# Performance work log

Hardware: AMD Instinct MI355X
Metric: run time of the kernel (lower is better)

## Reference

```python
import jax, jax.numpy as jnp
import numpy as np

D_MODEL = 1024
N_HEAD = 16
D_QKV = 64
B, L = 2, 2048
LN_EPS = 1e-5


def setup_inputs() -> dict:
    key = jax.random.key(0)
    ks = jax.random.split(key, 5)
    # xavier-normal-ish scale for [H, d_model, d_qkv] params
    std_in = (2.0 / (D_MODEL + D_QKV)) ** 0.5
    return {
        "x": jax.random.normal(ks[0], (B, L, D_MODEL), jnp.float32),
        "w_q": jax.random.normal(ks[1], (N_HEAD, D_MODEL, D_QKV), jnp.float32) * std_in,
        "w_k": jax.random.normal(ks[2], (N_HEAD, D_MODEL, D_QKV), jnp.float32) * std_in,
        "w_v": jax.random.normal(ks[3], (N_HEAD, D_MODEL, D_QKV), jnp.float32) * std_in,
        "w_o": jax.random.normal(ks[4], (N_HEAD, D_QKV, D_MODEL), jnp.float32) * std_in,
        "ln_gamma": jnp.ones((D_MODEL,), jnp.float32),
        "ln_beta": jnp.zeros((D_MODEL,), jnp.float32),
    }


def reference(x, w_q, w_k, w_v, w_o, ln_gamma, ln_beta):
    # q,k,v: [B, H, L, d_qkv]
    q = jnp.einsum('hmq,blm->bhlq', w_q, x)
    k = jnp.einsum('hmq,blm->bhlq', w_k, x)
    v = jnp.einsum('hmq,blm->bhlq', w_v, x)
    # scores: [B, H, L, L]
    s = jnp.einsum('bhiq,bhjq->bhij', q, k) / (D_QKV ** 0.5)
    s = jax.nn.softmax(s, axis=-1)
    # (dropout disabled: eval-mode reference)
    att = jnp.einsum('bhij,bhjq->bhiq', s, v)          # [B, H, L, d_qkv]
    out = jnp.einsum('bhlq,hqm->blm', att, w_o)        # [B, L, d_model]
    y = x + out                                        # residual
    mu = jnp.mean(y, axis=-1, keepdims=True)
    var = jnp.var(y, axis=-1, keepdims=True)
    return (y - mu) * jax.lax.rsqrt(var + LN_EPS) * ln_gamma + ln_beta
```

## Files before the change

### kernel.cpp

```cpp
#include <hip/hip_runtime.h>
#include <hip/hip_bf16.h>
#include <cstdint>

#define B_      2
#define L_      2048
#define DM_     1024
#define H_      16
#define DQ_     64
#define LN_EPS  1e-5f
#define QSCALE  0.1803368801111204f

typedef unsigned short u16;
typedef unsigned int   u32;
typedef __attribute__((ext_vector_type(8)))  short short8;
typedef __attribute__((ext_vector_type(4)))  unsigned short u16x4;
typedef __attribute__((ext_vector_type(4)))  unsigned int   u32x4;
typedef __attribute__((ext_vector_type(4)))  float f32x4;
typedef __attribute__((ext_vector_type(16))) float f32x16;

__device__ __forceinline__ u16 f2b(float f) {
  __hip_bfloat16 h = __float2bfloat16(f);
  return *reinterpret_cast<u16*>(&h);
}
__device__ __forceinline__ u32 pk2(float lo, float hi) {
  return (u32)f2b(lo) | ((u32)f2b(hi) << 16);
}

__device__ __forceinline__ void gl_lds16(const void* g, void* l) {
  auto gp = reinterpret_cast<const __attribute__((address_space(1))) unsigned int*>(
      reinterpret_cast<uintptr_t>(g));
  auto lp = reinterpret_cast<__attribute__((address_space(3))) unsigned int*>(
      reinterpret_cast<uintptr_t>(l));
  __builtin_amdgcn_global_load_lds(gp, lp, 16, 0, 0);
}

__device__ __forceinline__ short8 frag8(const u16* base, int row, int lchunk) {
  return *(const short8*)(base + row * 64 + ((lchunk ^ (row & 7)) << 3));
}

__global__ __launch_bounds__(256) void prep_all(
    const float* __restrict__ x, const float* __restrict__ wq,
    const float* __restrict__ wk, const float* __restrict__ wv,
    const float* __restrict__ wo, u16* __restrict__ xb,
    u16* __restrict__ wt, u16* __restrict__ wot) {
  __shared__ float Ls[64][65];
  const int t = threadIdx.x;
  const int bx = blockIdx.x;
  if (bx < 4096) {
    int i = bx * 256 + t;
    float4 v = ((const float4*)x)[i];
    u16x4 o = { f2b(v.x), f2b(v.y), f2b(v.z), f2b(v.w) };
    *(u16x4*)(xb + (size_t)i * 4) = o;
  } else if (bx < 4096 + 768) {
    int b2 = bx - 4096;
    int mt = b2 & 15, h = (b2 >> 4) & 15, wh = b2 >> 8;
    const float* in = ((wh == 0) ? wq : (wh == 1) ? wk : wv) + (size_t)h * DM_ * DQ_;
    #pragma unroll
    for (int i = 0; i < 16; ++i) {
      int idx = i * 256 + t, r = idx >> 6, c = idx & 63;
      Ls[r][c] = in[(size_t)(mt * 64 + r) * DQ_ + c];
    }
    __syncthreads();
    u16* outb = wt + (size_t)(wh * H_ + h) * DQ_ * DM_;
    #pragma unroll
    for (int i = 0; i < 16; ++i) {
      int idx = i * 256 + t, q = idx >> 6, mm = idx & 63;
      outb[(size_t)q * DM_ + mt * 64 + mm] = f2b(Ls[mm][q]);
    }
  } else {
    int b3 = bx - 4864;
    int mt = b3 & 15, kt = b3 >> 4;
    #pragma unroll
    for (int i = 0; i < 16; ++i) {
      int idx = i * 256 + t, r = idx >> 6, c = idx & 63;
      Ls[r][c] = wo[(size_t)(kt * 64 + r) * DM_ + mt * 64 + c];
    }
    __syncthreads();
    #pragma unroll
    for (int i = 0; i < 16; ++i) {
      int idx = i * 256 + t, mm = idx >> 6, kk = idx & 63;
      wot[(size_t)(mt * 64 + mm) * DM_ + kt * 64 + kk] = f2b(Ls[kk][mm]);
    }
  }
}

__global__ __launch_bounds__(256) void qkv_big(const u16* __restrict__ xb,
    const u16* __restrict__ wt, u16* __restrict__ Q, u16* __restrict__ K,
    u16* __restrict__ Vtg) {
  const int nt = blockIdx.x, mt = blockIdx.y;
  __shared__ __align__(16) u16 SH[128 * 136];
  u16* As_ = SH;
  u16* Bs_ = SH + 8192;
  const int t = threadIdx.x, w = t >> 6, lane = t & 63;
  const int lx = lane & 15, lq = lane >> 4;
  const int row0 = mt * 128, n0 = nt * 128;
  const int r8 = lane >> 3, lc = (lane & 7) ^ r8;
  const int wr = (w >> 1) * 64, wc = (w & 1) * 64;

  const u16* gA = xb + (size_t)(row0 + w * 32 + r8) * DM_ + lc * 8;
  const u16* gB = wt + (size_t)(n0  + w * 32 + r8) * DM_ + lc * 8;
  u16* lA = As_ + (w * 32) * 64;
  u16* lB = Bs_ + (w * 32) * 64;

  f32x4 z = {0.f, 0.f, 0.f, 0.f};
  f32x4 acc[4][4];
  #pragma unroll
  for (int mb = 0; mb < 4; ++mb)
    #pragma unroll
    for (int nb = 0; nb < 4; ++nb) acc[mb][nb] = z;

  for (int k0 = 0; k0 < DM_; k0 += 64) {
    #pragma unroll
    for (int i = 0; i < 4; ++i) {
      gl_lds16(gA + (size_t)i * 8 * DM_ + k0, lA + i * 8 * 64);
      gl_lds16(gB + (size_t)i * 8 * DM_ + k0, lB + i * 8 * 64);
    }
    __syncthreads();
    short8 af[4][2];
    #pragma unroll
    for (int mb = 0; mb < 4; ++mb)
      #pragma unroll
      for (int kh = 0; kh < 2; ++kh)
        af[mb][kh] = frag8(As_, wr + mb * 16 + lx, (kh << 2) | lq);
    #pragma unroll
    for (int nb = 0; nb < 4; ++nb) {
      short8 b0 = frag8(Bs_, wc + nb * 16 + lx, lq);
      short8 b1 = frag8(Bs_, wc + nb * 16 + lx, 4 | lq);
      #pragma unroll
      for (int mb = 0; mb < 4; ++mb) {
        acc[mb][nb] = __builtin_amdgcn_mfma_f32_16x16x32_bf16(af[mb][0], b0, acc[mb][nb], 0, 0, 0);
        acc[mb][nb] = __builtin_amdgcn_mfma_f32_16x16x32_bf16(af[mb][1], b1, acc[mb][nb], 0, 0, 0);
      }
    }
    __syncthreads();
  }

  const int wh = n0 >> 10;
  const float oscale = (wh == 0) ? QSCALE : 1.0f;
  const int bb = row0 >> 11, l0 = row0 & 2047;
  const int hd0 = n0 & 1023;
  u16* Ep = SH;

  if (wh != 2) {
    #pragma unroll
    for (int mb = 0; mb < 4; ++mb)
      #pragma unroll
      for (int nb = 0; nb < 4; ++nb)
        #pragma unroll
        for (int r = 0; r < 4; ++r) {
          int l = wr + mb * 16 + lq * 4 + r;
          Ep[l * 136 + wc + nb * 16 + lx] = f2b(acc[mb][nb][r] * oscale);
        }
    __syncthreads();
    u16* outp = (wh == 0) ? Q : K;
    #pragma unroll
    for (int hs = 0; hs < 2; ++hs) {
      const int hh = (hd0 >> 6) + hs;
      u16* gbase = outp + ((size_t)(bb * H_ + hh) * L_ + l0) * DQ_;
      #pragma unroll
      for (int it = 0; it < 4; ++it) {
        int u = it * 256 + t;
        int l = u >> 3, chunk = u & 7;
        *(uint4*)(gbase + u * 8) = *(const uint4*)&Ep[l * 136 + hs * 64 + chunk * 8];
      }
    }
  } else {
    #pragma unroll
    for (int mb = 0; mb < 4; ++mb)
      #pragma unroll
      for (int nb = 0; nb < 4; ++nb) {
        int l = wr + mb * 16 + lq * 4;
        int lp = (l & ~12) | ((l & 4) << 1) | ((l & 8) >> 1);
        uint2 pv = { pk2(acc[mb][nb][0], acc[mb][nb][1]),
                     pk2(acc[mb][nb][2], acc[mb][nb][3]) };
        *(uint2*)&Ep[(wc + nb * 16 + lx) * 136 + lp] = pv;
      }
    __syncthreads();
    #pragma unroll
    for (int it = 0; it < 8; ++it) {
      int v = it * 256 + t;
      int dloc = v >> 4, chunk = v & 15;
      int hh = (hd0 + dloc) >> 6, dd = (hd0 + dloc) & 63;
      u16* g = Vtg + ((size_t)(bb * H_ + hh) * DQ_ + dd) * L_ + l0 + chunk * 8;
      *(uint4*)g = *(const uint4*)&Ep[dloc * 136 + chunk * 8];
    }
  }
}

__global__ __launch_bounds__(512) void attn_mfma(const u16* __restrict__ Q,
    const u16* __restrict__ K, const u16* __restrict__ Vtg, u16* __restrict__ att) {
  const int ord = blockIdx.x;
  const int r_  = ord & 7, s_ = ord >> 3;
  const int qt  = s_ & 7, ghi = s_ >> 3;
  const int grp = r_ + 8 * ghi;
  const int h   = grp & 15, b = grp >> 4;
  __shared__ __align__(16) u16 Qs_[256 * 64];
  __shared__ __align__(16) u16 Ks_[2][64 * 64];
  __shared__ __align__(16) u16 Vt_[2][64 * 64];
  const int t = threadIdx.x, w = t >> 6, lane = t & 63;
  const int c = lane & 31, lsel = lane >> 5;
  const int r8 = lane >> 3, lc = (lane & 7) ^ r8;
  const size_t bh  = (size_t)(b * H_ + h) * L_ * DQ_;
  const size_t bhv = (size_t)(b * H_ + h) * DQ_ * L_;

  const u16* gQ = Q + bh + (size_t)(qt * 256 + w * 32 + r8) * DQ_ + lc * 8;
  #pragma unroll
  for (int i = 0; i < 4; ++i) gl_lds16(gQ + (size_t)i * 8 * DQ_, Qs_ + (w * 32 + i * 8) * 64);

  const u16* gK = K   + bh  + (size_t)(w * 8 + r8) * DQ_ + lc * 8;
  const u16* gV = Vtg + bhv + (size_t)(w * 8 + r8) * L_  + lc * 8;

  gl_lds16(gK, Ks_[0] + w * 8 * 64);
  gl_lds16(gV, Vt_[0] + w * 8 * 64);
  __syncthreads();
  short8 qb[4];
  #pragma unroll
  for (int km = 0; km < 4; ++km) qb[km] = frag8(Qs_, w * 32 + c, (km << 1) | lsel);

  f32x16 zz = {0.f,0.f,0.f,0.f,0.f,0.f,0.f,0.f,0.f,0.f,0.f,0.f,0.f,0.f,0.f,0.f};
  f32x16 oacc0 = zz, oacc1 = zz, lacc = zz;
  const short one_bf = (short)0x3F80;
  short8 ones = {one_bf, one_bf, one_bf, one_bf, one_bf, one_bf, one_bf, one_bf};

  for (int kt = 0; kt < L_ / 64; ++kt) {
    const int cur = kt & 1;
    __syncthreads();

    if (kt + 1 < L_ / 64) {
      const int nxt = 1 - cur;
      gl_lds16(gK + (size_t)(kt + 1) * 64 * DQ_, Ks_[nxt] + w * 8 * 64);
      gl_lds16(gV + (size_t)(kt + 1) * 64,       Vt_[nxt] + w * 8 * 64);
    }

    u32x4 paw[4];
    #pragma unroll
    for (int kb = 0; kb < 2; ++kb) {
      f32x16 s = zz;
      #pragma unroll
      for (int km = 0; km < 4; ++km) {
        short8 ka = frag8(Ks_[cur], kb * 32 + c, (km << 1) | lsel);
        s = __builtin_amdgcn_mfma_f32_32x32x16_bf16(ka, qb[km], s, 0, 0, 0);
      }
      #pragma unroll
      for (int F = 0; F < 2; ++F) {
        u32x4 pw;
        #pragma unroll
        for (int i = 0; i < 4; ++i) {
          float p0 = __builtin_amdgcn_exp2f(s[8 * F + 2 * i]);
          float p1 = __builtin_amdgcn_exp2f(s[8 * F + 2 * i + 1]);
          pw[i] = __builtin_amdgcn_perm(__float_as_uint(p1), __float_as_uint(p0), 0x07060302u);
        }
        paw[2 * kb + F] = pw;
      }
    }

    #pragma unroll
    for (int km = 0; km < 4; ++km) {
      short8 pa  = *reinterpret_cast<const short8*>(&paw[km]);
      short8 vb0 = frag8(Vt_[cur], c,      (km << 1) | lsel);
      short8 vb1 = frag8(Vt_[cur], 32 + c, (km << 1) | lsel);
      oacc0 = __builtin_amdgcn_mfma_f32_32x32x16_bf16(pa, vb0, oacc0, 0, 0, 0);
      oacc1 = __builtin_amdgcn_mfma_f32_32x32x16_bf16(pa, vb1, oacc1, 0, 0, 0);
      lacc  = __builtin_amdgcn_mfma_f32_32x32x16_bf16(pa, ones, lacc, 0, 0, 0);
    }
  }

  const int qrow_base = qt * 256 + w * 32;
  #pragma unroll
  for (int r = 0; r < 16; ++r) {
    int qr = (r & 3) + 8 * (r >> 2) + 4 * lsel;
    float inv = 1.0f / lacc[r];
    size_t base = (size_t)(b * L_ + qrow_base + qr) * DM_ + h * DQ_;
    att[base + c]      = f2b(oacc0[r] * inv);
    att[base + 32 + c] = f2b(oacc1[r] * inv);
  }
}

__global__ __launch_bounds__(256) void oproj_big(const u16* __restrict__ A,
    const u16* __restrict__ wot, float* __restrict__ out) {
  const int nt = blockIdx.x, mt = blockIdx.y;
  __shared__ __align__(16) u16 As_[128 * 64];
  __shared__ __align__(16) u16 Bs_[128 * 64];
  const int t = threadIdx.x, w = t >> 6, lane = t & 63;
  const int lx = lane & 15, lq = lane >> 4;
  const int row0 = mt * 128, n0 = nt * 128;
  const int r8 = lane >> 3, lc = (lane & 7) ^ r8;
  const int wr = (w >> 1) * 64, wc = (w & 1) * 64;

  const u16* gA = A   + (size_t)(row0 + w * 32 + r8) * DM_ + lc * 8;
  const u16* gB = wot + (size_t)(n0  + w * 32 + r8) * DM_ + lc * 8;
  u16* lA = As_ + (w * 32) * 64;
  u16* lB = Bs_ + (w * 32) * 64;

  f32x4 z = {0.f, 0.f, 0.f, 0.f};
  f32x4 acc[4][4];
  #pragma unroll
  for (int mb = 0; mb < 4; ++mb)
    #pragma unroll
    for (int nb = 0; nb < 4; ++nb) acc[mb][nb] = z;

  for (int k0 = 0; k0 < DM_; k0 += 64) {
    #pragma unroll
    for (int i = 0; i < 4; ++i) {
      gl_lds16(gA + (size_t)i * 8 * DM_ + k0, lA + i * 8 * 64);
      gl_lds16(gB + (size_t)i * 8 * DM_ + k0, lB + i * 8 * 64);
    }
    __syncthreads();
    short8 af[4][2];
    #pragma unroll
    for (int mb = 0; mb < 4; ++mb)
      #pragma unroll
      for (int kh = 0; kh < 2; ++kh)
        af[mb][kh] = frag8(As_, wr + mb * 16 + lx, (kh << 2) | lq);
    #pragma unroll
    for (int nb = 0; nb < 4; ++nb) {
      short8 b0 = frag8(Bs_, wc + nb * 16 + lx, lq);
      short8 b1 = frag8(Bs_, wc + nb * 16 + lx, 4 | lq);
      #pragma unroll
      for (int mb = 0; mb < 4; ++mb) {
        acc[mb][nb] = __builtin_amdgcn_mfma_f32_16x16x32_bf16(af[mb][0], b0, acc[mb][nb], 0, 0, 0);
        acc[mb][nb] = __builtin_amdgcn_mfma_f32_16x16x32_bf16(af[mb][1], b1, acc[mb][nb], 0, 0, 0);
      }
    }
    __syncthreads();
  }
  #pragma unroll
  for (int mb = 0; mb < 4; ++mb)
    #pragma unroll
    for (int nb = 0; nb < 4; ++nb)
      #pragma unroll
      for (int r = 0; r < 4; ++r) {
        int row = row0 + wr + mb * 16 + lq * 4 + r;
        out[(size_t)row * DM_ + n0 + wc + nb * 16 + lx] = acc[mb][nb][r];
      }
}

__global__ __launch_bounds__(256) void resid_ln(
    const float* __restrict__ x, const float* __restrict__ gamma,
    const float* __restrict__ beta, float* __restrict__ out) {
  const int row = blockIdx.x;
  const int t   = threadIdx.x;
  const float4* xp = (const float4*)(x   + (size_t)row * DM_);
  float4*       yp = (float4*)      (out + (size_t)row * DM_);

  float4 xv = xp[t];
  float4 av = yp[t];
  float y0 = xv.x + av.x, y1 = xv.y + av.y, y2 = xv.z + av.z, y3 = xv.w + av.w;

  float s  = y0 + y1 + y2 + y3;
  float s2 = y0 * y0 + y1 * y1 + y2 * y2 + y3 * y3;
  #pragma unroll
  for (int off = 32; off > 0; off >>= 1) {
    s  += __shfl_xor(s,  off, 64);
    s2 += __shfl_xor(s2, off, 64);
  }
  __shared__ float red[8];
  const int wave = t >> 6, lane = t & 63;
  if (lane == 0) { red[wave] = s; red[4 + wave] = s2; }
  __syncthreads();
  s  = red[0] + red[1] + red[2] + red[3];
  s2 = red[4] + red[5] + red[6] + red[7];

  const float mean = s * (1.f / DM_);
  const float var  = s2 * (1.f / DM_) - mean * mean;
  const float inv  = rsqrtf(var + LN_EPS);

  const float4 g  = ((const float4*)gamma)[t];
  const float4 bt = ((const float4*)beta)[t];
  float4 r;
  r.x = (y0 - mean) * inv * g.x + bt.x;
  r.y = (y1 - mean) * inv * g.y + bt.y;
  r.z = (y2 - mean) * inv * g.z + bt.z;
  r.w = (y3 - mean) * inv * g.w + bt.w;
  yp[t] = r;
}

extern "C" void kernel_launch(void* const* d_in, const int* in_sizes, int n_in,
                              void* d_out, int out_size, void* d_ws, size_t ws_size,
                              hipStream_t stream) {
  const float* x     = (const float*)d_in[0];
  const float* wq    = (const float*)d_in[1];
  const float* wk    = (const float*)d_in[2];
  const float* wv    = (const float*)d_in[3];
  const float* wo    = (const float*)d_in[4];
  const float* gamma = (const float*)d_in[5];
  const float* beta  = (const float*)d_in[6];
  float* out = (float*)d_out;

  char* ws = (char*)d_ws;
  u16* xb  = (u16*)ws;
  u16* Qb  = (u16*)(ws + ((size_t)8  << 20));
  u16* Kb  = (u16*)(ws + ((size_t)16 << 20));
  u16* Vtg = (u16*)(ws + ((size_t)24 << 20));
  u16* wt  = (u16*)(ws + ((size_t)32 << 20));
  u16* wot = (u16*)(ws + ((size_t)38 << 20));
  u16* att = (u16*)(ws + ((size_t)40 << 20));

  prep_all <<<5120, 256, 0, stream>>>(x, wq, wk, wv, wo, xb, wt, wot);
  qkv_big  <<<dim3(24, 32),    256, 0, stream>>>(xb, wt, Qb, Kb, Vtg);
  attn_mfma<<<256, 512, 0, stream>>>(Qb, Kb, Vtg, att);
  oproj_big<<<dim3(8, 32),     256, 0, stream>>>(att, wot, out);
  resid_ln <<<B_ * L_, 256, 0, stream>>>(x, gamma, beta, out);
}
```

Baseline: 186.3 us.

## Double-buffer QKV GEMM with 256x256 tiles, 512 threads and block swizzle

The QKV projection GEMM moves from 128x128 tiles with 256 threads and a single LDS buffer to 256x256 tiles with 512 threads and two LDS buffers. Global-to-LDS loads for the next K-step are issued during the MFMA work, synchronised with explicit vmcnt waits and raw s_barrier. A block-index swizzle is added for cache locality, and the epilogue is done in two halves to fit LDS. This aims to hide load latency and raise data reuse, at the cost of fewer blocks (192 on a 256-CU part), more registers per thread, and 128KB of LDS.

```diff
diff --git a/kernel.cpp b/kernel.cpp
--- a/kernel.cpp
+++ b/kernel.cpp
@@ -33,6 +33,8 @@
       reinterpret_cast<uintptr_t>(l));
   __builtin_amdgcn_global_load_lds(gp, lp, 16, 0, 0);
 }
+
+__device__ __forceinline__ void bar() { asm volatile("s_barrier" ::: "memory"); }
 
 __device__ __forceinline__ short8 frag8(const u16* base, int row, int lchunk) {
   return *(const short8*)(base + row * 64 + ((lchunk ^ (row & 7)) << 3));
@@ -84,105 +86,154 @@
   }
 }
 
-__global__ __launch_bounds__(256) void qkv_big(const u16* __restrict__ xb,
+__global__ __launch_bounds__(512) void qkv_big(const u16* __restrict__ xb,
     const u16* __restrict__ wt, u16* __restrict__ Q, u16* __restrict__ K,
     u16* __restrict__ Vtg) {
-  const int nt = blockIdx.x, mt = blockIdx.y;
-  __shared__ __align__(16) u16 SH[128 * 136];
-  u16* As_ = SH;
-  u16* Bs_ = SH + 8192;
+  const int raw = blockIdx.x;
+  const int swz = (raw & 7) * 24 + (raw >> 3);
+  const int nt = swz >> 4, mt = swz & 15;
+  __shared__ __align__(16) u16 SH[65536];
+  u16* const A0 = SH;
+  u16* const B0 = SH + 16384;
+  u16* const A1 = SH + 32768;
+  u16* const B1 = SH + 49152;
   const int t = threadIdx.x, w = t >> 6, lane = t & 63;
   const int lx = lane & 15, lq = lane >> 4;
-  const int row0 = mt * 128, n0 = nt * 128;
   const int r8 = lane >> 3, lc = (lane & 7) ^ r8;
-  const int wr = (w >> 1) * 64, wc = (w & 1) * 64;
+  const int row0 = mt * 256, n0 = nt * 256;
+  const int wr = (w >> 2) * 128, wc = (w & 3) * 64;
 
   const u16* gA = xb + (size_t)(row0 + w * 32 + r8) * DM_ + lc * 8;
   const u16* gB = wt + (size_t)(n0  + w * 32 + r8) * DM_ + lc * 8;
-  u16* lA = As_ + (w * 32) * 64;
-  u16* lB = Bs_ + (w * 32) * 64;
+  const int lw = (w * 32) * 64;
+
+  #pragma unroll
+  for (int s = 0; s < 4; ++s)
+    gl_lds16(gA + (size_t)s * 8 * DM_, A0 + lw + s * 8 * 64);
+  #pragma unroll
+  for (int s = 0; s < 4; ++s)
+    gl_lds16(gB + (size_t)s * 8 * DM_, B0 + lw + s * 8 * 64);
+  gl_lds16(gA + 64 + (size_t)0 * 8 * DM_, A1 + lw + 0 * 8 * 64);
+  gl_lds16(gA + 64 + (size_t)1 * 8 * DM_, A1 + lw + 1 * 8 * 64);
+  asm volatile("s_waitcnt vmcnt(2)" ::: "memory");
+  bar();
 
   f32x4 z = {0.f, 0.f, 0.f, 0.f};
-  f32x4 acc[4][4];
-  #pragma unroll
-  for (int mb = 0; mb < 4; ++mb)
-    #pragma unroll
-    for (int nb = 0; nb < 4; ++nb) acc[mb][nb] = z;
-
-  for (int k0 = 0; k0 < DM_; k0 += 64) {
-    #pragma unroll
-    for (int i = 0; i < 4; ++i) {
-      gl_lds16(gA + (size_t)i * 8 * DM_ + k0, lA + i * 8 * 64);
-      gl_lds16(gB + (size_t)i * 8 * DM_ + k0, lB + i * 8 * 64);
-    }
-    __syncthreads();
-    short8 af[4][2];
-    #pragma unroll
-    for (int mb = 0; mb < 4; ++mb)
-      #pragma unroll
-      for (int kh = 0; kh < 2; ++kh)
-        af[mb][kh] = frag8(As_, wr + mb * 16 + lx, (kh << 2) | lq);
-    #pragma unroll
-    for (int nb = 0; nb < 4; ++nb) {
-      short8 b0 = frag8(Bs_, wc + nb * 16 + lx, lq);
-      short8 b1 = frag8(Bs_, wc + nb * 16 + lx, 4 | lq);
-      #pragma unroll
-      for (int mb = 0; mb < 4; ++mb) {
-        acc[mb][nb] = __builtin_amdgcn_mfma_f32_16x16x32_bf16(af[mb][0], b0, acc[mb][nb], 0, 0, 0);
-        acc[mb][nb] = __builtin_amdgcn_mfma_f32_16x16x32_bf16(af[mb][1], b1, acc[mb][nb], 0, 0, 0);
-      }
-    }
-    __syncthreads();
-  }
-
-  const int wh = n0 >> 10;
+  f32x4 acc[8][4];
+  #pragma unroll
+  for (int mf = 0; mf < 8; ++mf)
+    #pragma unroll
+    for (int nf = 0; nf < 4; ++nf) acc[mf][nf] = z;
+
+  for (int tau = 0; tau < 16; ++tau) {
+    const int d = tau & 1;
+    u16* Ad = d ? A1 : A0;
+    u16* Bd = d ? B1 : B0;
+    u16* Ao = d ? A0 : A1;
+    u16* Bo = d ? B0 : B1;
+    const int t1 = (tau + 1 < 16) ? tau + 1 : 15;
+
+    short8 af[8], bf[4];
+    #pragma unroll
+    for (int mf = 0; mf < 8; ++mf) af[mf] = frag8(Ad, wr + mf * 16 + lx, lq);
+    #pragma unroll
+    for (int nf = 0; nf < 4; ++nf) bf[nf] = frag8(Bd, wc + nf * 16 + lx, lq);
+
+    gl_lds16(gA + (size_t)t1 * 64 + (size_t)2 * 8 * DM_, Ao + lw + 2 * 8 * 64);
+    gl_lds16(gA + (size_t)t1 * 64 + (size_t)3 * 8 * DM_, Ao + lw + 3 * 8 * 64);
+    #pragma unroll
+    for (int s = 0; s < 4; ++s)
+      gl_lds16(gB + (size_t)t1 * 64 + (size_t)s * 8 * DM_, Bo + lw + s * 8 * 64);
+
+    #pragma unroll
+    for (int nf = 0; nf < 4; ++nf)
+      #pragma unroll
+      for (int mf = 0; mf < 8; ++mf)
+        acc[mf][nf] = __builtin_amdgcn_mfma_f32_16x16x32_bf16(af[mf], bf[nf], acc[mf][nf], 0, 0, 0);
+
+    #pragma unroll
+    for (int mf = 0; mf < 8; ++mf) af[mf] = frag8(Ad, wr + mf * 16 + lx, 4 | lq);
+    #pragma unroll
+    for (int nf = 0; nf < 4; ++nf) bf[nf] = frag8(Bd, wc + nf * 16 + lx, 4 | lq);
+    #pragma unroll
+    for (int nf = 0; nf < 4; ++nf)
+      #pragma unroll
+      for (int mf = 0; mf < 8; ++mf)
+        acc[mf][nf] = __builtin_amdgcn_mfma_f32_16x16x32_bf16(af[mf], bf[nf], acc[mf][nf], 0, 0, 0);
+
+    bar();
+
+    const int t2 = (tau + 2 < 16) ? tau + 2 : 15;
+    gl_lds16(gA + (size_t)t2 * 64 + (size_t)0 * 8 * DM_, Ad + lw + 0 * 8 * 64);
+    gl_lds16(gA + (size_t)t2 * 64 + (size_t)1 * 8 * DM_, Ad + lw + 1 * 8 * 64);
+
+    asm volatile("s_waitcnt vmcnt(2)" ::: "memory");
+    bar();
+  }
+  asm volatile("s_waitcnt vmcnt(0)" ::: "memory");
+  bar();
+
+  const int wh  = nt >> 2;
   const float oscale = (wh == 0) ? QSCALE : 1.0f;
-  const int bb = row0 >> 11, l0 = row0 & 2047;
-  const int hd0 = n0 & 1023;
+  const int bb  = row0 >> 11, l0 = row0 & 2047;
+  const int hd0 = (nt & 3) * 256;
   u16* Ep = SH;
 
   if (wh != 2) {
-    #pragma unroll
-    for (int mb = 0; mb < 4; ++mb)
-      #pragma unroll
-      for (int nb = 0; nb < 4; ++nb)
+    u16* outp = (wh == 0) ? Q : K;
+    #pragma unroll
+    for (int mp = 0; mp < 2; ++mp) {
+      if ((w >> 2) == mp) {
         #pragma unroll
-        for (int r = 0; r < 4; ++r) {
-          int l = wr + mb * 16 + lq * 4 + r;
-          Ep[l * 136 + wc + nb * 16 + lx] = f2b(acc[mb][nb][r] * oscale);
+        for (int mf = 0; mf < 8; ++mf)
+          #pragma unroll
+          for (int nf = 0; nf < 4; ++nf)
+            #pragma unroll
+            for (int r = 0; r < 4; ++r) {
+              int l = mf * 16 + lq * 4 + r;
+              Ep[l * 264 + wc + nf * 16 + lx] = f2b(acc[mf][nf][r] * oscale);
+            }
+      }
+      __syncthreads();
+      #pragma unroll
+      for (int hs = 0; hs < 4; ++hs) {
+        const int hh = (hd0 >> 6) + hs;
+        u16* gbase = outp + ((size_t)(bb * H_ + hh) * L_ + l0 + mp * 128) * DQ_;
+        #pragma unroll
+        for (int it = 0; it < 2; ++it) {
+          int u = it * 512 + t;
+          int l = u >> 3, ch = u & 7;
+          *(uint4*)(gbase + (size_t)u * 8) = *(const uint4*)&Ep[l * 264 + hs * 64 + ch * 8];
         }
-    __syncthreads();
-    u16* outp = (wh == 0) ? Q : K;
-    #pragma unroll
-    for (int hs = 0; hs < 2; ++hs) {
-      const int hh = (hd0 >> 6) + hs;
-      u16* gbase = outp + ((size_t)(bb * H_ + hh) * L_ + l0) * DQ_;
-      #pragma unroll
-      for (int it = 0; it < 4; ++it) {
-        int u = it * 256 + t;
-        int l = u >> 3, chunk = u & 7;
-        *(uint4*)(gbase + u * 8) = *(const uint4*)&Ep[l * 136 + hs * 64 + chunk * 8];
-      }
+      }
+      __syncthreads();
     }
   } else {
     #pragma unroll
-    for (int mb = 0; mb < 4; ++mb)
-      #pragma unroll
-      for (int nb = 0; nb < 4; ++nb) {
-        int l = wr + mb * 16 + lq * 4;
-        int lp = (l & ~12) | ((l & 4) << 1) | ((l & 8) >> 1);
-        uint2 pv = { pk2(acc[mb][nb][0], acc[mb][nb][1]),
-                     pk2(acc[mb][nb][2], acc[mb][nb][3]) };
-        *(uint2*)&Ep[(wc + nb * 16 + lx) * 136 + lp] = pv;
-      }
-    __syncthreads();
-    #pragma unroll
-    for (int it = 0; it < 8; ++it) {
-      int v = it * 256 + t;
-      int dloc = v >> 4, chunk = v & 15;
-      int hh = (hd0 + dloc) >> 6, dd = (hd0 + dloc) & 63;
-      u16* g = Vtg + ((size_t)(bb * H_ + hh) * DQ_ + dd) * L_ + l0 + chunk * 8;
-      *(uint4*)g = *(const uint4*)&Ep[dloc * 136 + chunk * 8];
+    for (int mp = 0; mp < 2; ++mp) {
+      if ((w >> 2) == mp) {
+        #pragma unroll
+        for (int mf = 0; mf < 8; ++mf)
+          #pragma unroll
+          for (int nf = 0; nf < 4; ++nf) {
+            int ll = mf * 16 + lq * 4;
+            int lp = (ll & ~12) | ((ll & 4) << 1) | ((ll & 8) >> 1);
+            int dd = wc + nf * 16 + lx;
+            uint2 pv = { pk2(acc[mf][nf][0], acc[mf][nf][1]),
+                         pk2(acc[mf][nf][2], acc[mf][nf][3]) };
+            *(uint2*)&Ep[dd * 136 + lp] = pv;
+          }
+      }
+      __syncthreads();
+      #pragma unroll
+      for (int it = 0; it < 8; ++it) {
+        int v = it * 512 + t;
+        int dloc = v >> 4, ch = v & 15;
+        int hh = (hd0 + dloc) >> 6, ddg = (hd0 + dloc) & 63;
+        u16* g = Vtg + ((size_t)(bb * H_ + hh) * DQ_ + ddg) * L_ + l0 + mp * 128 + ch * 8;
+        *(uint4*)g = *(const uint4*)&Ep[dloc * 136 + ch * 8];
+      }
+      __syncthreads();
     }
   }
 }
@@ -397,8 +448,8 @@
   u16* att = (u16*)(ws + ((size_t)40 << 20));
 
   prep_all <<<5120, 256, 0, stream>>>(x, wq, wk, wv, wo, xb, wt, wot);
-  qkv_big  <<<dim3(24, 32),    256, 0, stream>>>(xb, wt, Qb, Kb, Vtg);
+  qkv_big  <<<192, 512, 0, stream>>>(xb, wt, Qb, Kb, Vtg);
   attn_mfma<<<256, 512, 0, stream>>>(Qb, Kb, Vtg, att);
-  oproj_big<<<dim3(8, 32),     256, 0, stream>>>(att, wot, out);
+  oproj_big<<<dim3(8, 32), 256, 0, stream>>>(att, wot, out);
   resid_ln <<<B_ * L_, 256, 0, stream>>>(x, gamma, beta, out);
 }
```

New measurement: 184.1 us (median of 2 runs). No clear change (-1.2%).
